# Optimization experiments

Hardware: AMD Instinct MI355X
Metric: run time of the kernel (lower is better)

The kernel has to match this reference:

```python
import jax, jax.numpy as jnp
import numpy as np


def _rms(x, w=None, eps=1e-6):
    # RMSNorm in fp32 like the torch module, optional elementwise affine.
    x32 = x.astype(jnp.float32)
    r = jax.lax.rsqrt(jnp.mean(x32 * x32, axis=-1, keepdims=True) + eps)
    y = (x32 * r).astype(x.dtype)
    return y * w if w is not None else y


def _rotate_half(x):
    x1, x2 = jnp.split(x, 2, axis=-1)
    return jnp.concatenate([-x2, x1], axis=-1)


def setup_inputs() -> dict:
    key = jax.random.key(0)
    ks = jax.random.split(key, 10)
    B, N, C, H = 16, 1024, 1152, 16
    hd = C // H          # 72
    hid = 3072           # _swiglu_hidden(1152, 4.0)
    grid = 32            # grid**2 == N
    quarter = hd // 4    # 18
    # exact axial RoPE cache (build_axial_rope_cache)
    inv_freq = 1.0 / (10000.0 ** (np.arange(quarter, dtype=np.float32) / quarter))
    pos = np.arange(grid, dtype=np.float32)
    f1 = pos[:, None] * inv_freq[None, :]                               # (grid, quarter)
    fy = np.broadcast_to(f1[:, None, :], (grid, grid, quarter)).reshape(-1, quarter)
    fx = np.broadcast_to(f1[None, :, :], (grid, grid, quarter)).reshape(-1, quarter)

    def cs(f):
        e = np.concatenate([f, f], axis=-1)                             # (N, hd//2)
        return jnp.asarray(np.cos(e))[None, None], jnp.asarray(np.sin(e))[None, None]

    cos_y, sin_y = cs(fy)
    cos_x, sin_x = cs(fx)

    def w(k, shp, scale=0.02):
        return jax.random.normal(k, shp, jnp.float32) * scale

    return {
        "x": jax.random.normal(ks[0], (B, N, C), jnp.float32),
        "temb": jax.random.normal(ks[1], (B, C), jnp.float32),
        "cos_y": cos_y, "sin_y": sin_y, "cos_x": cos_x, "sin_x": sin_x,
        "Wqkv": w(ks[2], (3 * C, C)), "bqkv": jnp.zeros((3 * C,), jnp.float32),
        "Wt": w(ks[3], (3 * C, C)), "bt": jnp.zeros((3 * C,), jnp.float32),
        "Wp": w(ks[4], (C, C)), "bp": jnp.zeros((C,), jnp.float32),
        "qn_w": jnp.ones((hd,), jnp.float32), "kn_w": jnp.ones((hd,), jnp.float32),
        "Wg": w(ks[5], (hid, C)), "bg": jnp.zeros((hid,), jnp.float32),
        "Wu": w(ks[6], (hid, C)), "bu": jnp.zeros((hid,), jnp.float32),
        "Wd": w(ks[7], (C, hid)), "bd": jnp.zeros((C,), jnp.float32),
    }


def reference(x, temb, cos_y, sin_y, cos_x, sin_x, Wqkv, bqkv, Wt, bt, Wp, bp,
              qn_w, kn_w, Wg, bg, Wu, bu, Wd, bd):
    B, N, C = x.shape
    H = 16
    hd = C // H

    # --- TMSA attention branch ---
    xn = _rms(x)                                            # norm1 (no affine)
    qkv = xn @ Wqkv.T + bqkv + (temb @ Wt.T + bt)[:, None, :]
    qkv = qkv.reshape(B, N, 3, H, hd).transpose(2, 0, 3, 1, 4)  # (3,B,H,N,hd)
    q, k, v = qkv[0], qkv[1], qkv[2]
    q = _rms(q, qn_w)
    k = _rms(k, kn_w)

    def rope(t):
        ty, tx = jnp.split(t, 2, axis=-1)
        ty = ty * cos_y + _rotate_half(ty) * sin_y
        tx = tx * cos_x + _rotate_half(tx) * sin_x
        return jnp.concatenate([ty, tx], axis=-1)

    q, k = rope(q), rope(k)

    scores = jnp.einsum('bhnd,bhmd->bhnm', q, k) / jnp.sqrt(jnp.float32(hd))
    attn = jax.nn.softmax(scores, axis=-1)
    o = jnp.einsum('bhnm,bhmd->bhnd', attn, v)
    o = o.transpose(0, 2, 1, 3).reshape(B, N, C)
    x = x + (o @ Wp.T + bp)

    # --- SwiGLU MLP branch ---
    xn2 = _rms(x)                                           # norm2 (no affine)
    h = jax.nn.silu(xn2 @ Wg.T + bg) * (xn2 @ Wu.T + bu)
    x = x + (h @ Wd.T + bd)
    return x
```

## Files before the change

### kernel.cpp

```cpp
#include <hip/hip_runtime.h>
#include <cstdint>
#include <cstddef>

typedef unsigned short u16;
typedef unsigned int u32;
typedef __attribute__((ext_vector_type(8))) short bf16x8s;
typedef __attribute__((ext_vector_type(4))) float f32x4;

#define ASG __attribute__((address_space(1)))
#define ASL __attribute__((address_space(3)))

__device__ __forceinline__ u16 f2bf(float f){
  union { float f; unsigned u; } v; v.f = f;
  unsigned r = v.u + 0x7FFFu + ((v.u >> 16) & 1u);
  return (u16)(r >> 16);
}
__device__ __forceinline__ float bf2f(u16 h){
  union { unsigned u; float f; } v; v.u = ((unsigned)h) << 16;
  return v.f;
}

__global__ __launch_bounds__(256) void cvt_kernel(const float* __restrict__ in,
                                                  u16* __restrict__ out, int n){
  int i = blockIdx.x*256 + threadIdx.x;
  if (i < n) out[i] = f2bf(in[i]);
}

__global__ __launch_bounds__(256) void cvt_gu_kernel(const float* __restrict__ Wg,
                                                     const float* __restrict__ Wu,
                                                     u16* __restrict__ out){
  size_t i = (size_t)blockIdx.x*256 + threadIdx.x;
  if (i >= (size_t)6144*1152) return;
  int j = (int)(i / 1152), k = (int)(i % 1152);
  int b16 = j >> 4, w = j & 15;
  int src = (b16 >> 1)*16 + w;
  const float* W = (b16 & 1) ? Wu : Wg;
  out[i] = f2bf(W[(size_t)src*1152 + k]);
}

__global__ __launch_bounds__(256) void temb_kernel(const float* __restrict__ temb,
                                                   const float* __restrict__ Wt,
                                                   const float* __restrict__ bt,
                                                   const float* __restrict__ bqkv,
                                                   float* __restrict__ tvec){
  const int col  = blockIdx.x*4 + (threadIdx.x>>6);
  const int lane = threadIdx.x & 63;
  const float* wp = Wt + (size_t)col*1152;
  float w[18];
  #pragma unroll
  for (int j=0;j<18;j++) w[j] = wp[lane + j*64];
  float acc[16];
  #pragma unroll
  for (int b=0;b<16;b++) acc[b] = 0.f;
  #pragma unroll
  for (int j=0;j<18;j++){
    const int k = lane + j*64;
    #pragma unroll
    for (int b=0;b<16;b++) acc[b] += w[j]*temb[b*1152 + k];
  }
  #pragma unroll
  for (int b=0;b<16;b++){
    #pragma unroll
    for (int d=1; d<64; d<<=1) acc[b] += __shfl_xor(acc[b], d);
  }
  if (lane == 0){
    float add = bt[col] + bqkv[col];
    #pragma unroll
    for (int b=0;b<16;b++) tvec[(size_t)b*3456 + col] = acc[b] + add;
  }
}

__global__ __launch_bounds__(256) void rms_kernel(const float* __restrict__ in,
                                                  u16* __restrict__ out, int C){
  int row = blockIdx.x;
  const float* p = in + (size_t)row*C;
  float ss = 0.f;
  for (int c = threadIdx.x; c < C; c += 256){ float v = p[c]; ss += v*v; }
  #pragma unroll
  for (int d=1; d<64; d<<=1) ss += __shfl_xor(ss, d);
  __shared__ float wsum[4];
  if ((threadIdx.x & 63) == 0) wsum[threadIdx.x>>6] = ss;
  __syncthreads();
  float tot = wsum[0]+wsum[1]+wsum[2]+wsum[3];
  float r = rsqrtf(tot/(float)C + 1e-6f);
  u16* o = out + (size_t)row*C;
  for (int c = threadIdx.x; c < C; c += 256) o[c] = f2bf(p[c]*r);
}

template<int MODE>
__global__ __launch_bounds__(512, 4) void gemm_kernel(
    const u16* __restrict__ A, const u16* __restrict__ B,
    int M, int N, int K, int nbx, int segw,
    const float* __restrict__ bias, const float* __restrict__ fextra,
    void* __restrict__ outv, u16* __restrict__ out2, u16* __restrict__ out3)
{
  __shared__ __align__(16) u16 As0[256*32];
  __shared__ __align__(16) u16 As1[256*32];
  __shared__ __align__(16) u16 As2[256*32];
  __shared__ __align__(16) u16 Bs0[128*32];
  __shared__ __align__(16) u16 Bs1[128*32];
  __shared__ __align__(16) u16 Bs2[128*32];
  const int tid  = threadIdx.x;
  const int lane = tid & 63;
  const int wv   = tid >> 6;
  const int wr   = wv >> 1, wc = wv & 1;

  const int nwg  = (int)gridDim.x;
  const int bid  = (int)blockIdx.x;
  const int xcd  = bid & 7;
  const int slot = bid >> 3;
  const int mdep = (nwg >> 3) / nbx;
  const int segsz = mdep * segw;
  const int seg  = slot / segsz;
  const int rem  = slot - seg*segsz;
  const int mi   = rem / segw;
  const int ni   = seg*segw + (rem - mi*segw);
  const long m0 = (long)(xcd*mdep + mi) * 256;
  const long n0 = (long)ni * 128;

  const u16* Ab = A + (size_t)m0*K;
  const u16* Bb = B + (size_t)n0*K;

  const int gsw  = ((lane&3) ^ ((lane>>3)&3)) * 8;
  const int srow = lane >> 2;

  f32x4 acc[4][4];
  #pragma unroll
  for (int i=0;i<4;i++)
    #pragma unroll
    for (int j=0;j<4;j++) acc[i][j] = (f32x4){0.f,0.f,0.f,0.f};

  auto stage = [&](u16* as, u16* bs, int kt){
    __builtin_amdgcn_global_load_lds(
      (const ASG void*)(Ab + (size_t)(wv*16 + srow)*K + kt + gsw),
      (ASL void*)(as + wv*512), 16, 0, 0);
    __builtin_amdgcn_global_load_lds(
      (const ASG void*)(Ab + (size_t)(128 + wv*16 + srow)*K + kt + gsw),
      (ASL void*)(as + 4096 + wv*512), 16, 0, 0);
    __builtin_amdgcn_global_load_lds(
      (const ASG void*)(Bb + (size_t)(wv*16 + srow)*K + kt + gsw),
      (ASL void*)(bs + wv*512), 16, 0, 0);
  };
  auto compute = [&](const u16* as, const u16* bs){
    const int swc = (((lane>>4) ^ ((lane>>1)&3))) * 8;
    const int lc16 = lane & 15;
    bf16x8s af[4], bfr[4];
    #pragma unroll
    for (int i=0;i<4;i++)
      af[i] = *(const bf16x8s*)(as + (wr*64 + i*16 + lc16)*32 + swc);
    #pragma unroll
    for (int j=0;j<4;j++)
      bfr[j] = *(const bf16x8s*)(bs + (wc*64 + j*16 + lc16)*32 + swc);
    #pragma unroll
    for (int i=0;i<4;i++)
      #pragma unroll
      for (int j=0;j<4;j++)
        acc[i][j] = __builtin_amdgcn_mfma_f32_16x16x32_bf16(af[i], bfr[j], acc[i][j], 0,0,0);
  };

  const int NT = K >> 5;
  stage(As0, Bs0, 0);
  stage(As1, Bs1, 32);
  asm volatile("s_waitcnt vmcnt(3)" ::: "memory");
  __builtin_amdgcn_s_barrier();
  __builtin_amdgcn_sched_barrier(0);

  for (int t = 0; t < NT; t += 3){
    if (t+2 < NT) stage(As2, Bs2, (t+2)*32);
    compute(As0, Bs0);
    if (t+2 < NT) asm volatile("s_waitcnt vmcnt(3)" ::: "memory");
    else          asm volatile("s_waitcnt vmcnt(0)" ::: "memory");
    __builtin_amdgcn_s_barrier();
    __builtin_amdgcn_sched_barrier(0);
    if (t+3 < NT) stage(As0, Bs0, (t+3)*32);
    compute(As1, Bs1);
    if (t+3 < NT) asm volatile("s_waitcnt vmcnt(3)" ::: "memory");
    else          asm volatile("s_waitcnt vmcnt(0)" ::: "memory");
    __builtin_amdgcn_s_barrier();
    __builtin_amdgcn_sched_barrier(0);
    if (t+4 < NT) stage(As1, Bs1, (t+4)*32);
    compute(As2, Bs2);
    if (t+4 < NT) asm volatile("s_waitcnt vmcnt(3)" ::: "memory");
    else          asm volatile("s_waitcnt vmcnt(0)" ::: "memory");
    __builtin_amdgcn_s_barrier();
    __builtin_amdgcn_sched_barrier(0);
  }

  const int lr = (lane>>4)*4, lc = lane&15;
  #pragma unroll
  for (int i=0;i<4;i++){
    #pragma unroll
    for (int j=0;j<4;j++){
      long colg = n0 + wc*64 + j*16 + lc;
      long rowg0 = m0 + wr*64 + i*16 + lr;
      if (MODE==0){
        int cg = (int)colg;
        int which = cg / 1152;
        int rem2 = cg - which*1152;
        int hh = rem2 / 72, dd = rem2 - hh*72;
        int b = (int)(rowg0 >> 10), n = (int)(rowg0 & 1023);
        size_t bh = (size_t)(b*16 + hh);
        float tadd = fextra[(size_t)b*3456 + colg];
        if (which == 2){
          ushort4 vv;
          vv.x = f2bf(acc[i][j][0] + tadd);
          vv.y = f2bf(acc[i][j][1] + tadd);
          vv.z = f2bf(acc[i][j][2] + tadd);
          vv.w = f2bf(acc[i][j][3] + tadd);
          *(ushort4*)(out3 + (bh*72 + dd)*1024 + n) = vv;
        } else {
          u16* dst = (which==0) ? (u16*)outv : out2;
          #pragma unroll
          for (int r=0;r<4;r++)
            dst[(bh*1024 + (size_t)(n + r))*72 + dd] = f2bf(acc[i][j][r] + tadd);
        }
      } else {
        #pragma unroll
        for (int r=0;r<4;r++){
          long rowg = rowg0 + r;
          float v = acc[i][j][r];
          size_t oi = (size_t)rowg*N + colg;
          v += bias[colg] + fextra[oi];
          ((float*)outv)[oi] = v;
        }
      }
    }
  }
}

__global__ __launch_bounds__(512, 2) void gemm_gu8(
    const u16* __restrict__ A, const u16* __restrict__ B,
    int K, int nbx, int segw,
    const float* __restrict__ bg, const float* __restrict__ bu,
    u16* __restrict__ out)
{
  __shared__ __align__(16) u16 As0[256*64];
  __shared__ __align__(16) u16 Bs0[256*64];
  __shared__ __align__(16) u16 As1[256*64];
  __shared__ __align__(16) u16 Bs1[256*64];
  const int tid  = threadIdx.x;
  const int lane = tid & 63;
  const int wv   = tid >> 6;
  const int wr   = wv >> 2;
  const int wc   = wv & 3;
  const int g = lane >> 4, c = lane & 15;

  const int nwg  = (int)gridDim.x;
  const int bid  = (int)blockIdx.x;
  const int xcd  = bid & 7;
  const int slot = bid >> 3;
  const int mdep = (nwg >> 3) / nbx;
  const int segsz = mdep * segw;
  const int seg  = slot / segsz;
  const int rem  = slot - seg*segsz;
  const int mi   = rem / segw;
  const int ni   = seg*segw + (rem - mi*segw);
  const long m0 = (long)(xcd*mdep + mi) * 256;
  const long n0 = (long)ni * 256;

  const u16* Ab = A + (size_t)m0*K;
  const u16* Bb = B + (size_t)n0*K;

  const int srow = tid >> 3;
  const int q8   = ((tid & 7) ^ (srow & 7)) * 8;

  auto stageTo = [&](u16* dst, const u16* src, int h, int kt){
    __builtin_amdgcn_global_load_lds(
      (const ASG void*)(src + (size_t)(h*128 + srow)*K + kt + q8),
      (ASL void*)(dst + h*8192 + wv*512), 16, 0, 0);
    __builtin_amdgcn_global_load_lds(
      (const ASG void*)(src + (size_t)(h*128 + 64 + srow)*K + kt + q8),
      (ASL void*)(dst + h*8192 + 4096 + wv*512), 16, 0, 0);
  };

  f32x4 acc[8][4];
  #pragma unroll
  for (int i=0;i<8;i++)
    #pragma unroll
    for (int j=0;j<4;j++) acc[i][j] = (f32x4){0.f,0.f,0.f,0.f};

  const int sw0 = ((g     ) ^ (c & 7)) * 16;
  const int sw1 = ((4 + g ) ^ (c & 7)) * 16;

  const int NT = K >> 6;

  stageTo(As0, Ab, 0, 0);  stageTo(As0, Ab, 1, 0);
  stageTo(Bs0, Bb, 0, 0);  stageTo(Bs0, Bb, 1, 0);
  stageTo(Bs1, Bb, 0, 64); stageTo(Bs1, Bb, 1, 64);
  asm volatile("s_waitcnt vmcnt(4)" ::: "memory");
  __builtin_amdgcn_s_barrier();
  __builtin_amdgcn_sched_barrier(0);

  auto ktile = [&](const u16* CA, u16* CB, u16* NA, int t){
    const char* aB = (const char*)CA + wr*16384;
    const char* bB = (const char*)CB + (wc>>1)*16384;
    bf16x8s bfr[4][2];
    #pragma unroll
    for (int p=0;p<4;p++){
      const int r0 = (2*p)*16 + c;
      const int r1 = r0 + 16;
      bf16x8s a00 = *(const bf16x8s*)(aB + r0*128 + sw0);
      bf16x8s a01 = *(const bf16x8s*)(aB + r0*128 + sw1);
      bf16x8s a10 = *(const bf16x8s*)(aB + r1*128 + sw0);
      bf16x8s a11 = *(const bf16x8s*)(aB + r1*128 + sw1);
      if (p==0){
        #pragma unroll
        for (int j=0;j<4;j++){
          const int br = (wc&1)*64 + j*16 + c;
          bfr[j][0] = *(const bf16x8s*)(bB + br*128 + sw0);
          bfr[j][1] = *(const bf16x8s*)(bB + br*128 + sw1);
        }
        if (t+1 < NT) stageTo(NA, Ab, 0, (t+1)*64);
      } else if (p==1){
        if (t+1 < NT) stageTo(NA, Ab, 1, (t+1)*64);
      } else if (p==2){
        if (t+2 < NT) stageTo(CB, Bb, 0, (t+2)*64);
      } else {
        if (t+2 < NT) stageTo(CB, Bb, 1, (t+2)*64);
      }
      __builtin_amdgcn_s_barrier();
      asm volatile("s_waitcnt lgkmcnt(0)" ::: "memory");
      __builtin_amdgcn_sched_barrier(0);
      __builtin_amdgcn_s_setprio(1);
      #pragma unroll
      for (int j=0;j<4;j++){
        acc[2*p  ][j] = __builtin_amdgcn_mfma_f32_16x16x32_bf16(a00, bfr[j][0], acc[2*p  ][j],0,0,0);
        acc[2*p  ][j] = __builtin_amdgcn_mfma_f32_16x16x32_bf16(a01, bfr[j][1], acc[2*p  ][j],0,0,0);
        acc[2*p+1][j] = __builtin_amdgcn_mfma_f32_16x16x32_bf16(a10, bfr[j][0], acc[2*p+1][j],0,0,0);
        acc[2*p+1][j] = __builtin_amdgcn_mfma_f32_16x16x32_bf16(a11, bfr[j][1], acc[2*p+1][j],0,0,0);
      }
      __builtin_amdgcn_s_setprio(0);
      if (p==3){
        if (t+2 < NT) asm volatile("s_waitcnt vmcnt(4)" ::: "memory");
        else          asm volatile("s_waitcnt vmcnt(0)" ::: "memory");
      }
      __builtin_amdgcn_s_barrier();
      __builtin_amdgcn_sched_barrier(0);
    }
  };

  for (int tp = 0; tp < NT; tp += 2){
    ktile(As0, Bs0, As1, tp);
    ktile(As1, Bs1, As0, tp+1);
  }

  #pragma unroll
  for (int i=0;i<8;i++){
    #pragma unroll
    for (int jp=0;jp<2;jp++){
      long hcol = (n0>>1) + wc*32 + jp*16 + c;
      float bgv = bg[hcol], buv = bu[hcol];
      #pragma unroll
      for (int r=0;r<4;r++){
        long rowg = m0 + wr*128 + i*16 + g*4 + r;
        float gv = acc[i][2*jp  ][r] + bgv;
        float uv = acc[i][2*jp+1][r] + buv;
        float hv = (gv/(1.f + __expf(-gv))) * uv;
        out[(size_t)rowg*3072 + hcol] = f2bf(hv);
      }
    }
  }
}

__global__ __launch_bounds__(256) void qkrope_kernel(
    u16* __restrict__ Q, u16* __restrict__ K,
    const float* __restrict__ qn_w, const float* __restrict__ kn_w,
    const float* __restrict__ cos_y, const float* __restrict__ sin_y,
    const float* __restrict__ cos_x, const float* __restrict__ sin_x)
{
  const int gw   = blockIdx.x*4 + (threadIdx.x>>6);
  const int lane = threadIdx.x & 63;
  const int n = gw & 1023;
  const int d0 = lane*2;
  const bool act = d0 < 72;
  const float scale = 0.11785113019775793f;

  u16* qp = Q + (size_t)gw*72;
  u16* kp = K + (size_t)gw*72;
  float q0=0,q1=0,k0=0,k1=0,wq0=0,wq1=0,wk0=0,wk1=0;
  if (act){
    q0 = bf2f(qp[d0]); q1 = bf2f(qp[d0+1]);
    k0 = bf2f(kp[d0]); k1 = bf2f(kp[d0+1]);
    wq0 = qn_w[d0]; wq1 = qn_w[d0+1];
    wk0 = kn_w[d0]; wk1 = kn_w[d0+1];
  }
  float ssq = q0*q0 + q1*q1;
  float ssk = k0*k0 + k1*k1;
  #pragma unroll
  for (int d=1; d<64; d<<=1){ ssq += __shfl_xor(ssq,d); ssk += __shfl_xor(ssk,d); }
  const float rq = rsqrtf(ssq*(1.f/72.f) + 1e-6f);
  const float rk = rsqrtf(ssk*(1.f/72.f) + 1e-6f);
  float qn0 = q0*rq*wq0, qn1 = q1*rq*wq1;
  float kn0 = k0*rk*wk0, kn1 = k1*rk*wk1;

  int dh = d0 % 36;
  const bool first = (dh < 18);
  int partner = first ? lane+9 : lane-9;
  if (!act) partner = lane;
  float pq0 = __shfl(qn0, partner), pq1 = __shfl(qn1, partner);
  float pk0 = __shfl(kn0, partner), pk1 = __shfl(kn1, partner);
  if (act){
    const float* cp = (d0 < 36) ? cos_y : cos_x;
    const float* sp = (d0 < 36) ? sin_y : sin_x;
    float c0 = cp[n*36+dh], c1 = cp[n*36+dh+1];
    float s0 = sp[n*36+dh], s1 = sp[n*36+dh+1];
    float sgn = first ? -1.f : 1.f;
    float qo0 = (qn0*c0 + sgn*pq0*s0)*scale, qo1 = (qn1*c1 + sgn*pq1*s1)*scale;
    float ko0 = kn0*c0 + sgn*pk0*s0,         ko1 = kn1*c1 + sgn*pk1*s1;
    *(unsigned*)(qp + d0) = (unsigned)f2bf(qo0) | ((unsigned)f2bf(qo1)<<16);
    *(unsigned*)(kp + d0) = (unsigned)f2bf(ko0) | ((unsigned)f2bf(ko1)<<16);
  }
}

__global__ __launch_bounds__(256, 3) void attn_kernel(
    const u16* __restrict__ Q, const u16* __restrict__ K,
    const u16* __restrict__ Vt, u16* __restrict__ O)
{
  const int tid  = threadIdx.x;
  const int lane = tid & 63;
  const int wv   = tid >> 6;
  const int g = lane >> 4, c = lane & 15;
  const int bid  = blockIdx.x;
  const int head = (bid >> 6) * 8 + (bid & 7);
  const int q0   = ((bid >> 3) & 7) * 128;
  const int b = head >> 4, h = head & 15;

  __shared__ __align__(16) u16 Vlds[80][72];
  __shared__ __align__(16) u16 Plds[8][16][64];

  const bf16x8s zf = {0,0,0,0,0,0,0,0};
  const u16* Kp = K + (size_t)head*1024*72;
  const u16* Qb = Q + ((size_t)head*1024 + q0 + wv*32)*72;
  const char* Vg = (const char*)(Vt + (size_t)head*72*1024);

  bf16x8s qf[2][3];
  #pragma unroll
  for (int s=0;s<2;s++){
    const u16* qrow = Qb + (size_t)(s*16 + c)*72;
    qf[s][0] = *(const bf16x8s*)(qrow + g*8);
    qf[s][1] = *(const bf16x8s*)(qrow + 32 + g*8);
    qf[s][2] = (g==0) ? *(const bf16x8s*)(qrow + 64) : zf;
  }

  f32x4 oacc[2][5];
  float lsum[2] = {0.f, 0.f};
  #pragma unroll
  for (int s=0;s<2;s++)
    #pragma unroll
    for (int c5=0;c5<5;c5++) oacc[s][c5] = (f32x4){0.f,0.f,0.f,0.f};

  char* pb0 = (char*)Plds + (wv*2+0)*2048 + c*128;
  char* pb1 = pb0 + 2048;
  const int swz = (c & 7) << 4;

  int4 vr0, vr1, vr2;
  {
    vr0 = *(const int4*)(Vg + ((tid    )>>3)*2048 + ((tid    )&7)*16);
    vr1 = *(const int4*)(Vg + ((256+tid)>>3)*2048 + ((256+tid)&7)*16);
    if (tid < 64) vr2 = *(const int4*)(Vg + ((512+tid)>>3)*2048 + ((512+tid)&7)*16);
  }
  if (tid < 288) ((u32*)&Vlds[72][0])[tid] = 0u;
  {
    *(int4*)((char*)Vlds + ((tid    )>>3)*144 + ((tid    )&7)*16) = vr0;
    *(int4*)((char*)Vlds + ((256+tid)>>3)*144 + ((256+tid)&7)*16) = vr1;
    if (tid < 64) *(int4*)((char*)Vlds + ((512+tid)>>3)*144 + ((512+tid)&7)*16) = vr2;
  }

  for (int t = 0; t < 16; ++t){
    const int kv0 = t*64;
    __syncthreads();
    if (t < 15){
      const char* vs = Vg + (kv0+64)*2;
      vr0 = *(const int4*)(vs + ((tid    )>>3)*2048 + ((tid    )&7)*16);
      vr1 = *(const int4*)(vs + ((256+tid)>>3)*2048 + ((256+tid)&7)*16);
      if (tid < 64) vr2 = *(const int4*)(vs + ((512+tid)>>3)*2048 + ((512+tid)&7)*16);
    }

    #pragma unroll
    for (int nf=0; nf<4; nf++){
      const u16* krow = Kp + (size_t)(kv0 + nf*16 + c)*72;
      bf16x8s kf0 = *(const bf16x8s*)(krow + g*8);
      bf16x8s kf1 = *(const bf16x8s*)(krow + 32 + g*8);
      bf16x8s kf2 = (g==0) ? *(const bf16x8s*)(krow + 64) : zf;
      #pragma unroll
      for (int s=0;s<2;s++){
        f32x4 sc = (f32x4){0.f,0.f,0.f,0.f};
        sc = __builtin_amdgcn_mfma_f32_16x16x32_bf16(kf0, qf[s][0], sc,0,0,0);
        sc = __builtin_amdgcn_mfma_f32_16x16x32_bf16(kf1, qf[s][1], sc,0,0,0);
        sc = __builtin_amdgcn_mfma_f32_16x16x32_bf16(kf2, qf[s][2], sc,0,0,0);
        float p0 = __expf(sc[0]), p1 = __expf(sc[1]);
        float p2 = __expf(sc[2]), p3 = __expf(sc[3]);
        lsum[s] += (p0+p1) + (p2+p3);
        u32 w0 = (u32)f2bf(p0) | ((u32)f2bf(p1) << 16);
        u32 w1 = (u32)f2bf(p2) | ((u32)f2bf(p3) << 16);
        char* pb = s ? pb1 : pb0;
        int kb = nf*32 + g*8;
        *(u32*)(pb + ( kb      ^ swz)) = w0;
        *(u32*)(pb + ((kb + 4) ^ swz)) = w1;
      }
    }
    asm volatile("" ::: "memory");
    bf16x8s pa[2][2];
    #pragma unroll
    for (int s=0;s<2;s++)
      #pragma unroll
      for (int w2=0;w2<2;w2++)
        pa[s][w2] = *(const bf16x8s*)((s?pb1:pb0) + ((w2*64 + g*16) ^ swz));

    #pragma unroll
    for (int c5=0;c5<5;c5++){
      #pragma unroll
      for (int w2=0;w2<2;w2++){
        bf16x8s vf = *(const bf16x8s*)((const char*)Vlds + (size_t)(c5*16+c)*144 + w2*64 + g*16);
        oacc[0][c5] = __builtin_amdgcn_mfma_f32_16x16x32_bf16(pa[0][w2], vf, oacc[0][c5],0,0,0);
        oacc[1][c5] = __builtin_amdgcn_mfma_f32_16x16x32_bf16(pa[1][w2], vf, oacc[1][c5],0,0,0);
      }
    }

    if (t < 15){
      __syncthreads();
      *(int4*)((char*)Vlds + ((tid    )>>3)*144 + ((tid    )&7)*16) = vr0;
      *(int4*)((char*)Vlds + ((256+tid)>>3)*144 + ((256+tid)&7)*16) = vr1;
      if (tid < 64) *(int4*)((char*)Vlds + ((512+tid)>>3)*144 + ((512+tid)&7)*16) = vr2;
    }
  }

  size_t obase = (size_t)b*1024*1152 + (size_t)h*72;
  #pragma unroll
  for (int s=0;s<2;s++){
    float ls = lsum[s];
    ls += __shfl_xor(ls, 16);
    ls += __shfl_xor(ls, 32);
    float linv[4];
    #pragma unroll
    for (int r=0;r<4;r++) linv[r] = 1.0f / __shfl(ls, 4*g + r);
    #pragma unroll
    for (int c5=0;c5<5;c5++){
      int d = c5*16 + c;
      if (d < 72){
        #pragma unroll
        for (int r=0;r<4;r++){
          int n = q0 + wv*32 + s*16 + 4*g + r;
          O[obase + (size_t)n*1152 + d] = f2bf(oacc[s][c5][r]*linv[r]);
        }
      }
    }
  }
}

extern "C" void kernel_launch(void* const* d_in, const int* in_sizes, int n_in,
                              void* d_out, int out_size, void* d_ws, size_t ws_size,
                              hipStream_t stream) {
  const float* x    = (const float*)d_in[0];
  const float* temb = (const float*)d_in[1];
  const float* cos_y= (const float*)d_in[2];
  const float* sin_y= (const float*)d_in[3];
  const float* cos_x= (const float*)d_in[4];
  const float* sin_x= (const float*)d_in[5];
  const float* Wqkv = (const float*)d_in[6];
  const float* bqkv = (const float*)d_in[7];
  const float* Wt   = (const float*)d_in[8];
  const float* bt   = (const float*)d_in[9];
  const float* Wp   = (const float*)d_in[10];
  const float* bp   = (const float*)d_in[11];
  const float* qn_w = (const float*)d_in[12];
  const float* kn_w = (const float*)d_in[13];
  const float* Wg   = (const float*)d_in[14];
  const float* bg   = (const float*)d_in[15];
  const float* Wu   = (const float*)d_in[16];
  const float* bu   = (const float*)d_in[17];
  const float* Wd   = (const float*)d_in[18];
  const float* bd   = (const float*)d_in[19];

  char* ws = (char*)d_ws;
  size_t off = 0;
  auto alloc = [&](size_t bytes)->void*{
    off = (off + 255) & ~(size_t)255;
    void* p = ws + off; off += bytes; return p;
  };

  u16*   wbuf  = (u16*)alloc((size_t)6144*1152*2);
  float* tvec  = (float*)alloc((size_t)16*3456*4);
  u16*   xn_bf = (u16*)alloc((size_t)16384*1152*2);
  u16*   qt    = (u16*)alloc((size_t)262144*72*2);
  u16*   kt    = (u16*)alloc((size_t)262144*72*2);
  u16*   vt    = (u16*)alloc((size_t)256*72*1024*2);
  if (off > ws_size) return;

  u16*   o_bf   = xn_bf;
  u16*   xn2_bf = xn_bf;
  u16*   gbuf   = qt;
  float* x1     = (float*)d_out;

  rms_kernel<<<16384,256,0,stream>>>(x, xn_bf, 1152);
  temb_kernel<<<864,256,0,stream>>>(temb, Wt, bt, bqkv, tvec);

  cvt_kernel<<<(3456*1152+255)/256,256,0,stream>>>(Wqkv, wbuf, 3456*1152);
  gemm_kernel<0><<<64*27,512,0,stream>>>(
      xn_bf, wbuf, 16384, 3456, 1152, 27, 9, nullptr, tvec, qt, kt, vt);

  qkrope_kernel<<<65536,256,0,stream>>>(qt, kt, qn_w, kn_w, cos_y, sin_y, cos_x, sin_x);

  attn_kernel<<<2048,256,0,stream>>>(qt, kt, vt, o_bf);

  cvt_kernel<<<(1152*1152+255)/256,256,0,stream>>>(Wp, wbuf, 1152*1152);
  gemm_kernel<1><<<64*9,512,0,stream>>>(
      o_bf, wbuf, 16384, 1152, 1152, 9, 9, bp, x, x1, nullptr, nullptr);

  rms_kernel<<<16384,256,0,stream>>>(x1, xn2_bf, 1152);

  cvt_gu_kernel<<<(6144*1152+255)/256,256,0,stream>>>(Wg, Wu, wbuf);
  gemm_gu8<<<1536,512,0,stream>>>(
      xn2_bf, wbuf, 1152, 24, 4, bg, bu, gbuf);

  cvt_kernel<<<(1152*3072+255)/256,256,0,stream>>>(Wd, wbuf, 1152*3072);
  gemm_kernel<4><<<64*9,512,0,stream>>>(
      gbuf, wbuf, 16384, 1152, 3072, 9, 3, bd, x1, (float*)d_out, nullptr, nullptr);
}
```

Before: 1.004 ms.

## Switch GEMM kernels from 16x16x32 to 32x32x16 bf16 MFMA tiles

```diff
diff --git a/kernel.cpp b/kernel.cpp
--- a/kernel.cpp
+++ b/kernel.cpp
@@ -6,6 +6,7 @@
 typedef unsigned int u32;
 typedef __attribute__((ext_vector_type(8))) short bf16x8s;
 typedef __attribute__((ext_vector_type(4))) float f32x4;
+typedef __attribute__((ext_vector_type(16))) float f32x16;
 
 #define ASG __attribute__((address_space(1)))
 #define ASL __attribute__((address_space(3)))
@@ -32,9 +33,9 @@
   size_t i = (size_t)blockIdx.x*256 + threadIdx.x;
   if (i >= (size_t)6144*1152) return;
   int j = (int)(i / 1152), k = (int)(i % 1152);
-  int b16 = j >> 4, w = j & 15;
-  int src = (b16 >> 1)*16 + w;
-  const float* W = (b16 & 1) ? Wu : Wg;
+  int b32 = j >> 5, w = j & 31;
+  int src = (b32 >> 1)*32 + w;
+  const float* W = (b32 & 1) ? Wu : Wg;
   out[i] = f2bf(W[(size_t)src*1152 + k]);
 }
 
@@ -104,6 +105,7 @@
   const int lane = tid & 63;
   const int wv   = tid >> 6;
   const int wr   = wv >> 1, wc = wv & 1;
+  const int c32  = lane & 31, g2 = lane >> 5;
 
   const int nwg  = (int)gridDim.x;
   const int bid  = (int)blockIdx.x;
@@ -124,11 +126,13 @@
   const int gsw  = ((lane&3) ^ ((lane>>3)&3)) * 8;
   const int srow = lane >> 2;
 
-  f32x4 acc[4][4];
-  #pragma unroll
-  for (int i=0;i<4;i++)
-    #pragma unroll
-    for (int j=0;j<4;j++) acc[i][j] = (f32x4){0.f,0.f,0.f,0.f};
+  f32x16 acc[2][2];
+  #pragma unroll
+  for (int i=0;i<2;i++)
+    #pragma unroll
+    for (int j=0;j<2;j++)
+      #pragma unroll
+      for (int r=0;r<16;r++) acc[i][j][r] = 0.f;
 
   auto stage = [&](u16* as, u16* bs, int kt){
     __builtin_amdgcn_global_load_lds(
@@ -142,20 +146,23 @@
       (ASL void*)(bs + wv*512), 16, 0, 0);
   };
   auto compute = [&](const u16* as, const u16* bs){
-    const int swc = (((lane>>4) ^ ((lane>>1)&3))) * 8;
-    const int lc16 = lane & 15;
-    bf16x8s af[4], bfr[4];
-    #pragma unroll
-    for (int i=0;i<4;i++)
-      af[i] = *(const bf16x8s*)(as + (wr*64 + i*16 + lc16)*32 + swc);
-    #pragma unroll
-    for (int j=0;j<4;j++)
-      bfr[j] = *(const bf16x8s*)(bs + (wc*64 + j*16 + lc16)*32 + swc);
-    #pragma unroll
-    for (int i=0;i<4;i++)
-      #pragma unroll
-      for (int j=0;j<4;j++)
-        acc[i][j] = __builtin_amdgcn_mfma_f32_16x16x32_bf16(af[i], bfr[j], acc[i][j], 0,0,0);
+    const int xr = (c32 >> 1) & 3;
+    bf16x8s af[2][2], bfr[2][2];
+    #pragma unroll
+    for (int i=0;i<2;i++)
+      #pragma unroll
+      for (int s=0;s<2;s++){
+        int sl = (2*s + g2) ^ xr;
+        af[i][s]  = *(const bf16x8s*)(as + (wr*64 + i*32 + c32)*32 + sl*8);
+        bfr[i][s] = *(const bf16x8s*)(bs + (wc*64 + i*32 + c32)*32 + sl*8);
+      }
+    #pragma unroll
+    for (int i=0;i<2;i++)
+      #pragma unroll
+      for (int j=0;j<2;j++)
+        #pragma unroll
+        for (int s=0;s<2;s++)
+          acc[i][j] = __builtin_amdgcn_mfma_f32_32x32x16_bf16(af[i][s], bfr[j][s], acc[i][j],0,0,0);
   };
 
   const int NT = K >> 5;
@@ -186,41 +193,45 @@
     __builtin_amdgcn_sched_barrier(0);
   }
 
-  const int lr = (lane>>4)*4, lc = lane&15;
-  #pragma unroll
-  for (int i=0;i<4;i++){
-    #pragma unroll
-    for (int j=0;j<4;j++){
-      long colg = n0 + wc*64 + j*16 + lc;
-      long rowg0 = m0 + wr*64 + i*16 + lr;
+  #pragma unroll
+  for (int i=0;i<2;i++){
+    #pragma unroll
+    for (int j=0;j<2;j++){
+      long colg = n0 + wc*64 + j*32 + c32;
+      long rowbase = m0 + wr*64 + i*32;
       if (MODE==0){
         int cg = (int)colg;
         int which = cg / 1152;
         int rem2 = cg - which*1152;
         int hh = rem2 / 72, dd = rem2 - hh*72;
-        int b = (int)(rowg0 >> 10), n = (int)(rowg0 & 1023);
+        int b = (int)(rowbase >> 10), nb = (int)(rowbase & 1023);
         size_t bh = (size_t)(b*16 + hh);
         float tadd = fextra[(size_t)b*3456 + colg];
         if (which == 2){
-          ushort4 vv;
-          vv.x = f2bf(acc[i][j][0] + tadd);
-          vv.y = f2bf(acc[i][j][1] + tadd);
-          vv.z = f2bf(acc[i][j][2] + tadd);
-          vv.w = f2bf(acc[i][j][3] + tadd);
-          *(ushort4*)(out3 + (bh*72 + dd)*1024 + n) = vv;
+          #pragma unroll
+          for (int q=0;q<4;q++){
+            int n = nb + q*8 + g2*4;
+            ushort4 vv;
+            vv.x = f2bf(acc[i][j][4*q+0] + tadd);
+            vv.y = f2bf(acc[i][j][4*q+1] + tadd);
+            vv.z = f2bf(acc[i][j][4*q+2] + tadd);
+            vv.w = f2bf(acc[i][j][4*q+3] + tadd);
+            *(ushort4*)(out3 + (bh*72 + dd)*1024 + n) = vv;
+          }
         } else {
           u16* dst = (which==0) ? (u16*)outv : out2;
           #pragma unroll
-          for (int r=0;r<4;r++)
-            dst[(bh*1024 + (size_t)(n + r))*72 + dd] = f2bf(acc[i][j][r] + tadd);
+          for (int r=0;r<16;r++){
+            int n = nb + (r&3) + 8*(r>>2) + 4*g2;
+            dst[(bh*1024 + (size_t)n)*72 + dd] = f2bf(acc[i][j][r] + tadd);
+          }
         }
       } else {
         #pragma unroll
-        for (int r=0;r<4;r++){
-          long rowg = rowg0 + r;
-          float v = acc[i][j][r];
+        for (int r=0;r<16;r++){
+          long rowg = rowbase + (r&3) + 8*(r>>2) + 4*g2;
           size_t oi = (size_t)rowg*N + colg;
-          v += bias[colg] + fextra[oi];
+          float v = acc[i][j][r] + bias[colg] + fextra[oi];
           ((float*)outv)[oi] = v;
         }
       }
@@ -243,7 +254,7 @@
   const int wv   = tid >> 6;
   const int wr   = wv >> 2;
   const int wc   = wv & 3;
-  const int g = lane >> 4, c = lane & 15;
+  const int c32  = lane & 31, g2 = lane >> 5;
 
   const int nwg  = (int)gridDim.x;
   const int bid  = (int)blockIdx.x;
@@ -273,14 +284,15 @@
       (ASL void*)(dst + h*8192 + 4096 + wv*512), 16, 0, 0);
   };
 
-  f32x4 acc[8][4];
-  #pragma unroll
-  for (int i=0;i<8;i++)
-    #pragma unroll
-    for (int j=0;j<4;j++) acc[i][j] = (f32x4){0.f,0.f,0.f,0.f};
-
-  const int sw0 = ((g     ) ^ (c & 7)) * 16;
-  const int sw1 = ((4 + g ) ^ (c & 7)) * 16;
+  f32x16 acc[4][2];
+  #pragma unroll
+  for (int i=0;i<4;i++)
+    #pragma unroll
+    for (int j=0;j<2;j++)
+      #pragma unroll
+      for (int r=0;r<16;r++) acc[i][j][r] = 0.f;
+
+  const int x8 = c32 & 7;
 
   const int NT = K >> 6;
 
@@ -292,24 +304,25 @@
   __builtin_amdgcn_sched_barrier(0);
 
   auto ktile = [&](const u16* CA, u16* CB, u16* NA, int t){
-    const char* aB = (const char*)CA + wr*16384;
-    const char* bB = (const char*)CB + (wc>>1)*16384;
-    bf16x8s bfr[4][2];
+    const char* aB = (const char*)CA + (size_t)wr*128*128;
+    const char* bB = (const char*)CB;
+    bf16x8s bfr[2][4];
     #pragma unroll
     for (int p=0;p<4;p++){
-      const int r0 = (2*p)*16 + c;
-      const int r1 = r0 + 16;
-      bf16x8s a00 = *(const bf16x8s*)(aB + r0*128 + sw0);
-      bf16x8s a01 = *(const bf16x8s*)(aB + r0*128 + sw1);
-      bf16x8s a10 = *(const bf16x8s*)(aB + r1*128 + sw0);
-      bf16x8s a11 = *(const bf16x8s*)(aB + r1*128 + sw1);
+      bf16x8s a[4];
+      #pragma unroll
+      for (int s=0;s<4;s++){
+        int sl = (2*s + g2) ^ x8;
+        a[s] = *(const bf16x8s*)(aB + (size_t)(p*32 + c32)*128 + sl*16);
+      }
       if (p==0){
         #pragma unroll
-        for (int j=0;j<4;j++){
-          const int br = (wc&1)*64 + j*16 + c;
-          bfr[j][0] = *(const bf16x8s*)(bB + br*128 + sw0);
-          bfr[j][1] = *(const bf16x8s*)(bB + br*128 + sw1);
-        }
+        for (int j=0;j<2;j++)
+          #pragma unroll
+          for (int s=0;s<4;s++){
+            int sl = (2*s + g2) ^ x8;
+            bfr[j][s] = *(const bf16x8s*)(bB + (size_t)(wc*64 + j*32 + c32)*128 + sl*16);
+          }
         if (t+1 < NT) stageTo(NA, Ab, 0, (t+1)*64);
       } else if (p==1){
         if (t+1 < NT) stageTo(NA, Ab, 1, (t+1)*64);
@@ -323,11 +336,9 @@
       __builtin_amdgcn_sched_barrier(0);
       __builtin_amdgcn_s_setprio(1);
       #pragma unroll
-      for (int j=0;j<4;j++){
-        acc[2*p  ][j] = __builtin_amdgcn_mfma_f32_16x16x32_bf16(a00, bfr[j][0], acc[2*p  ][j],0,0,0);
-        acc[2*p  ][j] = __builtin_amdgcn_mfma_f32_16x16x32_bf16(a01, bfr[j][1], acc[2*p  ][j],0,0,0);
-        acc[2*p+1][j] = __builtin_amdgcn_mfma_f32_16x16x32_bf16(a10, bfr[j][0], acc[2*p+1][j],0,0,0);
-        acc[2*p+1][j] = __builtin_amdgcn_mfma_f32_16x16x32_bf16(a11, bfr[j][1], acc[2*p+1][j],0,0,0);
+      for (int s=0;s<4;s++){
+        acc[p][0] = __builtin_amdgcn_mfma_f32_32x32x16_bf16(a[s], bfr[0][s], acc[p][0],0,0,0);
+        acc[p][1] = __builtin_amdgcn_mfma_f32_32x32x16_bf16(a[s], bfr[1][s], acc[p][1],0,0,0);
       }
       __builtin_amdgcn_s_setprio(0);
       if (p==3){
@@ -344,20 +355,17 @@
     ktile(As1, Bs1, As0, tp+1);
   }
 
-  #pragma unroll
-  for (int i=0;i<8;i++){
-    #pragma unroll
-    for (int jp=0;jp<2;jp++){
-      long hcol = (n0>>1) + wc*32 + jp*16 + c;
-      float bgv = bg[hcol], buv = bu[hcol];
-      #pragma unroll
-      for (int r=0;r<4;r++){
-        long rowg = m0 + wr*128 + i*16 + g*4 + r;
-        float gv = acc[i][2*jp  ][r] + bgv;
-        float uv = acc[i][2*jp+1][r] + buv;
-        float hv = (gv/(1.f + __expf(-gv))) * uv;
-        out[(size_t)rowg*3072 + hcol] = f2bf(hv);
-      }
+  long hcol = (n0>>1) + wc*32 + c32;
+  float bgv = bg[hcol], buv = bu[hcol];
+  #pragma unroll
+  for (int i=0;i<4;i++){
+    #pragma unroll
+    for (int r=0;r<16;r++){
+      long rowg = m0 + wr*128 + i*32 + (r&3) + 8*(r>>2) + 4*g2;
+      float gv = acc[i][0][r] + bgv;
+      float uv = acc[i][1][r] + buv;
+      float hv = (gv/(1.f + __expf(-gv))) * uv;
+      out[(size_t)rowg*3072 + hcol] = f2bf(hv);
     }
   }
 }
```

Result: slower. 1.042 ms (+3.9%).

## Add 128x128 triple-buffered GEMM for output and down projections

Applied to the files above, without the earlier changes.

```diff
diff --git a/kernel.cpp b/kernel.cpp
--- a/kernel.cpp
+++ b/kernel.cpp
@@ -228,6 +228,125 @@
   }
 }
 
+template<int MODE>
+__global__ __launch_bounds__(256, 3) void gemm_half(
+    const u16* __restrict__ A, const u16* __restrict__ B,
+    int M, int N, int K, int nbx, int segw,
+    const float* __restrict__ bias, const float* __restrict__ fextra,
+    float* __restrict__ outv)
+{
+  __shared__ __align__(16) u16 As0[128*32];
+  __shared__ __align__(16) u16 As1[128*32];
+  __shared__ __align__(16) u16 As2[128*32];
+  __shared__ __align__(16) u16 Bs0[128*32];
+  __shared__ __align__(16) u16 Bs1[128*32];
+  __shared__ __align__(16) u16 Bs2[128*32];
+  const int tid  = threadIdx.x;
+  const int lane = tid & 63;
+  const int wv   = tid >> 6;
+  const int wr   = wv >> 1, wc = wv & 1;
+
+  const int nwg  = (int)gridDim.x;
+  const int bid  = (int)blockIdx.x;
+  const int xcd  = bid & 7;
+  const int slot = bid >> 3;
+  const int mdep = (nwg >> 3) / nbx;
+  const int segsz = mdep * segw;
+  const int seg  = slot / segsz;
+  const int rem  = slot - seg*segsz;
+  const int mi   = rem / segw;
+  const int ni   = seg*segw + (rem - mi*segw);
+  const long m0 = (long)(xcd*mdep + mi) * 128;
+  const long n0 = (long)ni * 128;
+
+  const u16* Ab = A + (size_t)m0*K;
+  const u16* Bb = B + (size_t)n0*K;
+
+  const int gsw  = ((lane&3) ^ ((lane>>3)&3)) * 8;
+  const int srow = lane >> 2;
+
+  f32x4 acc[4][4];
+  #pragma unroll
+  for (int i=0;i<4;i++)
+    #pragma unroll
+    for (int j=0;j<4;j++) acc[i][j] = (f32x4){0.f,0.f,0.f,0.f};
+
+  auto stage = [&](u16* as, u16* bs, int kt){
+    __builtin_amdgcn_global_load_lds(
+      (const ASG void*)(Ab + (size_t)(wv*16 + srow)*K + kt + gsw),
+      (ASL void*)(as + wv*512), 16, 0, 0);
+    __builtin_amdgcn_global_load_lds(
+      (const ASG void*)(Ab + (size_t)(64 + wv*16 + srow)*K + kt + gsw),
+      (ASL void*)(as + 2048 + wv*512), 16, 0, 0);
+    __builtin_amdgcn_global_load_lds(
+      (const ASG void*)(Bb + (size_t)(wv*16 + srow)*K + kt + gsw),
+      (ASL void*)(bs + wv*512), 16, 0, 0);
+    __builtin_amdgcn_global_load_lds(
+      (const ASG void*)(Bb + (size_t)(64 + wv*16 + srow)*K + kt + gsw),
+      (ASL void*)(bs + 2048 + wv*512), 16, 0, 0);
+  };
+  auto compute = [&](const u16* as, const u16* bs){
+    const int swc = (((lane>>4) ^ ((lane>>1)&3))) * 8;
+    const int lc16 = lane & 15;
+    bf16x8s af[4], bfr[4];
+    #pragma unroll
+    for (int i=0;i<4;i++)
+      af[i] = *(const bf16x8s*)(as + (wr*64 + i*16 + lc16)*32 + swc);
+    #pragma unroll
+    for (int j=0;j<4;j++)
+      bfr[j] = *(const bf16x8s*)(bs + (wc*64 + j*16 + lc16)*32 + swc);
+    #pragma unroll
+    for (int i=0;i<4;i++)
+      #pragma unroll
+      for (int j=0;j<4;j++)
+        acc[i][j] = __builtin_amdgcn_mfma_f32_16x16x32_bf16(af[i], bfr[j], acc[i][j], 0,0,0);
+  };
+
+  const int NT = K >> 5;
+  stage(As0, Bs0, 0);
+  stage(As1, Bs1, 32);
+  asm volatile("s_waitcnt vmcnt(4)" ::: "memory");
+  __builtin_amdgcn_s_barrier();
+  __builtin_amdgcn_sched_barrier(0);
+
+  for (int t = 0; t < NT; t += 3){
+    if (t+2 < NT) stage(As2, Bs2, (t+2)*32);
+    compute(As0, Bs0);
+    if (t+2 < NT) asm volatile("s_waitcnt vmcnt(4)" ::: "memory");
+    else          asm volatile("s_waitcnt vmcnt(0)" ::: "memory");
+    __builtin_amdgcn_s_barrier();
+    __builtin_amdgcn_sched_barrier(0);
+    if (t+3 < NT) stage(As0, Bs0, (t+3)*32);
+    compute(As1, Bs1);
+    if (t+3 < NT) asm volatile("s_waitcnt vmcnt(4)" ::: "memory");
+    else          asm volatile("s_waitcnt vmcnt(0)" ::: "memory");
+    __builtin_amdgcn_s_barrier();
+    __builtin_amdgcn_sched_barrier(0);
+    if (t+4 < NT) stage(As1, Bs1, (t+4)*32);
+    compute(As2, Bs2);
+    if (t+4 < NT) asm volatile("s_waitcnt vmcnt(4)" ::: "memory");
+    else          asm volatile("s_waitcnt vmcnt(0)" ::: "memory");
+    __builtin_amdgcn_s_barrier();
+    __builtin_amdgcn_sched_barrier(0);
+  }
+
+  const int lr = (lane>>4)*4, lc = lane&15;
+  #pragma unroll
+  for (int i=0;i<4;i++){
+    #pragma unroll
+    for (int j=0;j<4;j++){
+      long colg = n0 + wc*64 + j*16 + lc;
+      long rowg0 = m0 + wr*64 + i*16 + lr;
+      #pragma unroll
+      for (int r=0;r<4;r++){
+        long rowg = rowg0 + r;
+        size_t oi = (size_t)rowg*N + colg;
+        outv[oi] = acc[i][j][r] + bias[colg] + fextra[oi];
+      }
+    }
+  }
+}
+
 __global__ __launch_bounds__(512, 2) void gemm_gu8(
     const u16* __restrict__ A, const u16* __restrict__ B,
     int K, int nbx, int segw,
@@ -604,8 +723,8 @@
   attn_kernel<<<2048,256,0,stream>>>(qt, kt, vt, o_bf);
 
   cvt_kernel<<<(1152*1152+255)/256,256,0,stream>>>(Wp, wbuf, 1152*1152);
-  gemm_kernel<1><<<64*9,512,0,stream>>>(
-      o_bf, wbuf, 16384, 1152, 1152, 9, 9, bp, x, x1, nullptr, nullptr);
+  gemm_half<1><<<128*9,256,0,stream>>>(
+      o_bf, wbuf, 16384, 1152, 1152, 9, 9, bp, x, x1);
 
   rms_kernel<<<16384,256,0,stream>>>(x1, xn2_bf, 1152);
 
@@ -614,6 +733,6 @@
       xn2_bf, wbuf, 1152, 24, 4, bg, bu, gbuf);
 
   cvt_kernel<<<(1152*3072+255)/256,256,0,stream>>>(Wd, wbuf, 1152*3072);
-  gemm_kernel<4><<<64*9,512,0,stream>>>(
-      gbuf, wbuf, 16384, 1152, 3072, 9, 3, bd, x1, (float*)d_out, nullptr, nullptr);
-}
+  gemm_half<4><<<128*9,256,0,stream>>>(
+      gbuf, wbuf, 16384, 1152, 3072, 9, 3, bd, x1, (float*)d_out);
+}
```

Measured after the change: 983.6 us. 2.0% less time.
